# Kernel tuning notes

Hardware: AMD Instinct MI355X
Metric: run time of the kernel (lower is better)

## Reference

```python
import jax, jax.numpy as jnp
import numpy as np

B, C, H, W = 32, 384, 64, 64
M, R = 64, 16  # token_count, factor_r


def setup_inputs() -> dict:
    key = jax.random.key(0)
    k1, k2, k3, k4 = jax.random.split(key, 4)
    x = jax.random.normal(k1, (B, C, H, W), dtype=jnp.float32)
    # 1x1 conv == per-pixel linear map C -> R
    Vw = jax.random.normal(k2, (R, C), dtype=jnp.float32) * (1.0 / np.sqrt(C))
    Vb = jax.random.normal(k3, (R,), dtype=jnp.float32) * 0.01
    U = jax.random.normal(k4, (M, R), dtype=jnp.float32) * 0.02
    return {"x": x, "Vw": Vw, "Vb": Vb, "U": U}


def reference(x, Vw, Vb, U):
    b, c, h, w = x.shape
    n = h * w
    x_flat = x.reshape(b, c, n)                       # [B,C,N]
    # 1x1 conv projection: [B,R,N]
    V = jnp.einsum('rc,bcn->brn', Vw, x_flat) + Vb[None, :, None]
    # low-rank bilinear logits: [B,M,N]
    L = jnp.einsum('mr,brn->bmn', U, V)
    # softmax over token dim (axis=1), matching F.softmax(L, dim=1)
    S = jax.nn.softmax(L, axis=1)
    # pooled tokens: [B,C,M]
    T = jnp.einsum('bcn,bmn->bcm', x_flat, S)
    return (T, S)
```

## Files before the change

kernel.cpp:

```cpp
#include <hip/hip_runtime.h>
#include <hip/hip_bf16.h>

#define B_ 32
#define C_ 384
#define N_ 4096
#define M_ 64
#define R_ 16

typedef __attribute__((ext_vector_type(8))) short short8;
typedef __attribute__((ext_vector_type(4))) float f32x4;
typedef __attribute__((ext_vector_type(4))) int i32x4;

static __device__ __forceinline__ unsigned short f2bf(float f) {
    union { float f; unsigned u; } v; v.f = f;
    unsigned r = v.u + 0x7fffu + ((v.u >> 16) & 1u);
    return (unsigned short)(r >> 16);
}

__global__ __launch_bounds__(256) void k_w2(
    const float* __restrict__ Vw, const float* __restrict__ Vb,
    const float* __restrict__ U, unsigned short* __restrict__ W2,
    float* __restrict__ b2)
{
    __shared__ float vws[16 * 384];
    __shared__ float vbs[16];
    const int t = threadIdx.x;

    #pragma unroll
    for (int j = 0; j < 6; ++j)
        ((float4*)vws)[t + j * 256] = ((const float4*)Vw)[t + j * 256];
    if (t < 16) vbs[t] = Vb[t];
    __syncthreads();

    const int m  = blockIdx.x * 8 + (t >> 5);
    const int cg = t & 31;
    float u[R_];
    #pragma unroll
    for (int r = 0; r < R_; ++r) u[r] = U[m * R_ + r];
    if (cg == 0) {
        float a = 0.f;
        #pragma unroll
        for (int r = 0; r < R_; ++r) a = fmaf(u[r], vbs[r], a);
        b2[m] = a;
    }
    #pragma unroll
    for (int j = 0; j < 6; ++j) {
        const int c = cg * 2 + j * 64;
        float a0 = 0.f, a1 = 0.f;
        #pragma unroll
        for (int r = 0; r < R_; ++r) {
            float2 vv = *(const float2*)(vws + r * C_ + c);
            a0 = fmaf(u[r], vv.x, a0);
            a1 = fmaf(u[r], vv.y, a1);
        }
        unsigned pk = (unsigned)f2bf(a0) | ((unsigned)f2bf(a1) << 16);
        *(unsigned*)&W2[m * C_ + c] = pk;
    }
}

__global__ __launch_bounds__(512, 2) void k_fused(
    const float* __restrict__ x, const unsigned short* __restrict__ W2,
    const float* __restrict__ b2g, float* __restrict__ S, float* __restrict__ T)
{
    __shared__ unsigned short xcn[C_ * 128];
    __shared__ unsigned short xts[2][128][68];
    __shared__ unsigned short slds[M_ * 128];
    __shared__ float wred[2][4][128];

    const int t    = threadIdx.x;
    const int lane = t & 63;
    const int col  = lane & 15;
    const int q    = lane >> 4;
    const int w    = t >> 6;
    const int g    = w >> 1;
    const int h    = w & 1;

    const int b  = blockIdx.x >> 3;
    const int nq = blockIdx.x & 7;

    short8 af1[12];
    #pragma unroll
    for (int kk = 0; kk < 12; ++kk)
        af1[kk] = *(const short8*)(W2 + (g * 16 + col) * C_ + kk * 32 + q * 8);

    float bias[4];
    #pragma unroll
    for (int r = 0; r < 4; ++r) bias[r] = b2g[g * 16 + q * 4 + r];

    f32x4 acc2[3][4];
    #pragma unroll
    for (int ci = 0; ci < 3; ++ci)
        #pragma unroll
        for (int mt = 0; mt < 4; ++mt) acc2[ci][mt] = (f32x4){0.f, 0.f, 0.f, 0.f};

    const float* xb = x + (size_t)b * C_ * N_ + nq * 512 + 2 * lane;

    float2 xv[3][8];

    auto ISSUE = [&](float2 (&dst)[8], int subp, int kcp) {
        const float* xp = xb + (size_t)(kcp * 64 + w * 8) * N_ + subp * 128;
        #pragma unroll
        for (int i = 0; i < 8; ++i)
            dst[i] = *(const float2*)(xp + (size_t)i * N_);
    };

    auto CONVERT = [&](float2 (&v)[8], int kcp, int buf) {
        unsigned short bx[8], by[8];
        #pragma unroll
        for (int i = 0; i < 8; ++i) { bx[i] = f2bf(v[i].x); by[i] = f2bf(v[i].y); }
        #pragma unroll
        for (int i = 0; i < 8; ++i) {
            int c = kcp * 64 + w * 8 + i;
            unsigned pk = (unsigned)bx[i] | ((unsigned)by[i] << 16);
            *(unsigned*)((char*)xcn + c * 256 + ((lane * 4) ^ ((c & 7) << 4))) = pk;
        }
        i32x4 pa, pb;
        #pragma unroll
        for (int j = 0; j < 4; ++j) {
            pa[j] = (int)((unsigned)bx[2 * j] | ((unsigned)bx[2 * j + 1] << 16));
            pb[j] = (int)((unsigned)by[2 * j] | ((unsigned)by[2 * j + 1] << 16));
        }
        *(i32x4*)&xts[buf][2 * lane][w * 8]     = pa;
        *(i32x4*)&xts[buf][2 * lane + 1][w * 8] = pb;
    };

    ISSUE(xv[0], 0, 0);
    ISSUE(xv[1], 0, 1);
    ISSUE(xv[2], 0, 2);

    for (int sub = 0; sub < 4; ++sub) {
        f32x4 acc1[4];
        #pragma unroll
        for (int nt = 0; nt < 4; ++nt) acc1[nt] = (f32x4){0.f, 0.f, 0.f, 0.f};

        CONVERT(xv[0], 0, 0);
        __syncthreads();

        #pragma unroll
        for (int kc = 0; kc < 6; ++kc) {
            if (kc < 5) CONVERT(xv[(kc + 1) % 3], kc + 1, (kc + 1) & 1);
            if (kc < 3)          ISSUE(xv[kc % 3], sub, kc + 3);
            else if (sub < 3)    ISSUE(xv[kc % 3], sub + 1, kc - 3);

            #pragma unroll
            for (int ks = 0; ks < 2; ++ks) {
                short8 bfr[4];
                #pragma unroll
                for (int nt = 0; nt < 4; ++nt)
                    bfr[nt] = *(const short8*)&xts[kc & 1][h * 64 + nt * 16 + col][ks * 32 + q * 8];
                #pragma unroll
                for (int nt = 0; nt < 4; ++nt)
                    acc1[nt] = __builtin_amdgcn_mfma_f32_16x16x32_bf16(
                        af1[kc * 2 + ks], bfr[nt], acc1[nt], 0, 0, 0);
            }
            __syncthreads();
        }

        float mxl[4];
        #pragma unroll
        for (int nt = 0; nt < 4; ++nt) {
            float mx = -3.4e38f;
            #pragma unroll
            for (int r = 0; r < 4; ++r) {
                float vv = acc1[nt][r] + bias[r];
                acc1[nt][r] = vv;
                mx = fmaxf(mx, vv);
            }
            mx = fmaxf(mx, __shfl_xor(mx, 16, 64));
            mx = fmaxf(mx, __shfl_xor(mx, 32, 64));
            float s = 0.f;
            #pragma unroll
            for (int r = 0; r < 4; ++r) {
                float e = __expf(acc1[nt][r] - mx);
                acc1[nt][r] = e;
                s += e;
            }
            s += __shfl_xor(s, 16, 64);
            s += __shfl_xor(s, 32, 64);
            mxl[nt] = mx;
            if (q == 0) {
                int n = h * 64 + nt * 16 + col;
                wred[0][g][n] = mx;
                wred[1][g][n] = s;
            }
        }
        __syncthreads();

        float scl[4];
        #pragma unroll
        for (int nt = 0; nt < 4; ++nt) {
            int n = h * 64 + nt * 16 + col;
            float m0 = wred[0][0][n], m1 = wred[0][1][n];
            float m2 = wred[0][2][n], m3 = wred[0][3][n];
            float M  = fmaxf(fmaxf(m0, m1), fmaxf(m2, m3));
            float tot = wred[1][0][n] * __expf(m0 - M) + wred[1][1][n] * __expf(m1 - M)
                      + wred[1][2][n] * __expf(m2 - M) + wred[1][3][n] * __expf(m3 - M);
            scl[nt] = __expf(mxl[nt] - M) / tot;
        }

        float* Sp = S + (size_t)(b * M_ + g * 16 + q * 4) * N_ + nq * 512 + sub * 128;
        #pragma unroll
        for (int nt = 0; nt < 4; ++nt) {
            int n = h * 64 + nt * 16 + col;
            #pragma unroll
            for (int r = 0; r < 4; ++r) {
                float p = acc1[nt][r] * scl[nt];
                Sp[(size_t)r * N_ + n] = p;
                int m = g * 16 + q * 4 + r;
                *(unsigned short*)((char*)slds + m * 256 + ((2 * n) ^ ((m & 7) << 4))) = f2bf(p);
            }
        }
        __syncthreads();

        #pragma unroll
        for (int ks = 0; ks < 4; ++ks) {
            short8 a2[3], bsf[4];
            #pragma unroll
            for (int ci = 0; ci < 3; ++ci) {
                int c = w * 48 + ci * 16 + col;
                a2[ci] = *(const short8*)((char*)xcn + c * 256 +
                                          ((ks * 64 + q * 16) ^ ((c & 7) << 4)));
            }
            #pragma unroll
            for (int mt = 0; mt < 4; ++mt) {
                int m = mt * 16 + col;
                bsf[mt] = *(const short8*)((char*)slds + m * 256 +
                                           ((ks * 64 + q * 16) ^ ((m & 7) << 4)));
            }
            #pragma unroll
            for (int ci = 0; ci < 3; ++ci)
                #pragma unroll
                for (int mt = 0; mt < 4; ++mt)
                    acc2[ci][mt] = __builtin_amdgcn_mfma_f32_16x16x32_bf16(
                        a2[ci], bsf[mt], acc2[ci][mt], 0, 0, 0);
        }
        __syncthreads();
    }

    float* Tb = T + (size_t)b * C_ * M_;
    #pragma unroll
    for (int ci = 0; ci < 3; ++ci) {
        int c = w * 48 + ci * 16 + q * 4;
        #pragma unroll
        for (int mt = 0; mt < 4; ++mt)
            #pragma unroll
            for (int r = 0; r < 4; ++r)
                atomicAdd(&Tb[(size_t)(c + r) * M_ + mt * 16 + col], acc2[ci][mt][r]);
    }
}

extern "C" void kernel_launch(void* const* d_in, const int* in_sizes, int n_in,
                              void* d_out, int out_size, void* d_ws, size_t ws_size,
                              hipStream_t stream) {
    const float* x  = (const float*)d_in[0];
    const float* Vw = (const float*)d_in[1];
    const float* Vb = (const float*)d_in[2];
    const float* U  = (const float*)d_in[3];
    float* T = (float*)d_out;
    float* S = (float*)d_out + (size_t)B_ * C_ * M_;

    unsigned short* W2 = (unsigned short*)d_ws;
    float* b2 = (float*)((char*)d_ws + 64 * 384 * 2);

    hipMemsetAsync(T, 0, (size_t)B_ * C_ * M_ * sizeof(float), stream);
    k_w2<<<dim3(8), dim3(256), 0, stream>>>(Vw, Vb, U, W2, b2);
    k_fused<<<dim3(256), dim3(512), 0, stream>>>(x, W2, b2, S, T);
}
```

Before: 310.5 us.

## Halve pixel tile per block and double grid for higher occupancy

Each block now covers 256 pixels in sub-tiles of 64 instead of 512 in sub-tiles of 128, and the grid doubles to 512 blocks. Launch bounds ask for 4 blocks per SM instead of 2. The W2 fragments are reloaded from global or cache on every k-chunk rather than held in registers, and the x prefetch drops from triple to double buffering with a sync on every chunk. The goal is lower LDS and register use per block so more waves fit and latency is hidden, at the cost of more global W2 loads, more barriers and more T atomics.

```diff
diff --git a/kernel.cpp b/kernel.cpp
--- a/kernel.cpp
+++ b/kernel.cpp
@@ -58,30 +58,27 @@
     }
 }
 
-__global__ __launch_bounds__(512, 2) void k_fused(
+__global__ __launch_bounds__(512, 4) void k_fused(
     const float* __restrict__ x, const unsigned short* __restrict__ W2,
     const float* __restrict__ b2g, float* __restrict__ S, float* __restrict__ T)
 {
-    __shared__ unsigned short xcn[C_ * 128];
-    __shared__ unsigned short xts[2][128][68];
-    __shared__ unsigned short slds[M_ * 128];
-    __shared__ float wred[2][4][128];
+    __shared__ unsigned short xcn[C_ * 64];
+    __shared__ unsigned short xts[2][64][72];
+    __shared__ unsigned short slds[M_ * 64];
+    __shared__ float wred[2][4][64];
 
     const int t    = threadIdx.x;
     const int lane = t & 63;
     const int col  = lane & 15;
     const int q    = lane >> 4;
+    const int l31  = lane & 31;
+    const int l5   = lane >> 5;
     const int w    = t >> 6;
     const int g    = w >> 1;
     const int h    = w & 1;
 
-    const int b  = blockIdx.x >> 3;
-    const int nq = blockIdx.x & 7;
-
-    short8 af1[12];
-    #pragma unroll
-    for (int kk = 0; kk < 12; ++kk)
-        af1[kk] = *(const short8*)(W2 + (g * 16 + col) * C_ + kk * 32 + q * 8);
+    const int b  = blockIdx.x >> 4;
+    const int nq = blockIdx.x & 15;
 
     float bias[4];
     #pragma unroll
@@ -93,72 +90,72 @@
         #pragma unroll
         for (int mt = 0; mt < 4; ++mt) acc2[ci][mt] = (f32x4){0.f, 0.f, 0.f, 0.f};
 
-    const float* xb = x + (size_t)b * C_ * N_ + nq * 512 + 2 * lane;
-
-    float2 xv[3][8];
-
-    auto ISSUE = [&](float2 (&dst)[8], int subp, int kcp) {
-        const float* xp = xb + (size_t)(kcp * 64 + w * 8) * N_ + subp * 128;
-        #pragma unroll
-        for (int i = 0; i < 8; ++i)
-            dst[i] = *(const float2*)(xp + (size_t)i * N_);
+    const float* xb = x + (size_t)b * C_ * N_ + nq * 256 + 2 * l31;
+
+    float2 xv[2][4];
+
+    auto ISSUE = [&](float2 (&dst)[4], int subp, int kcp) {
+        const float* xp = xb + (size_t)(kcp * 64 + w * 8 + l5 * 4) * N_ + subp * 64;
+        #pragma unroll
+        for (int j = 0; j < 4; ++j)
+            dst[j] = *(const float2*)(xp + (size_t)j * N_);
     };
 
-    auto CONVERT = [&](float2 (&v)[8], int kcp, int buf) {
-        unsigned short bx[8], by[8];
-        #pragma unroll
-        for (int i = 0; i < 8; ++i) { bx[i] = f2bf(v[i].x); by[i] = f2bf(v[i].y); }
-        #pragma unroll
-        for (int i = 0; i < 8; ++i) {
-            int c = kcp * 64 + w * 8 + i;
-            unsigned pk = (unsigned)bx[i] | ((unsigned)by[i] << 16);
-            *(unsigned*)((char*)xcn + c * 256 + ((lane * 4) ^ ((c & 7) << 4))) = pk;
-        }
-        i32x4 pa, pb;
+    auto CONVERT = [&](float2 (&v)[4], int kcp, int buf) {
+        unsigned short bx[4], by[4];
+        #pragma unroll
+        for (int j = 0; j < 4; ++j) { bx[j] = f2bf(v[j].x); by[j] = f2bf(v[j].y); }
         #pragma unroll
         for (int j = 0; j < 4; ++j) {
-            pa[j] = (int)((unsigned)bx[2 * j] | ((unsigned)bx[2 * j + 1] << 16));
-            pb[j] = (int)((unsigned)by[2 * j] | ((unsigned)by[2 * j + 1] << 16));
-        }
-        *(i32x4*)&xts[buf][2 * lane][w * 8]     = pa;
-        *(i32x4*)&xts[buf][2 * lane + 1][w * 8] = pb;
+            int c = kcp * 64 + w * 8 + l5 * 4 + j;
+            unsigned pk = (unsigned)bx[j] | ((unsigned)by[j] << 16);
+            *(unsigned*)((char*)xcn + c * 128 + ((4 * l31) ^ ((c & 7) << 4))) = pk;
+        }
+        int cl = w * 8 + l5 * 4;
+        int2 pa, pb;
+        pa.x = (int)((unsigned)bx[0] | ((unsigned)bx[1] << 16));
+        pa.y = (int)((unsigned)bx[2] | ((unsigned)bx[3] << 16));
+        pb.x = (int)((unsigned)by[0] | ((unsigned)by[1] << 16));
+        pb.y = (int)((unsigned)by[2] | ((unsigned)by[3] << 16));
+        *(int2*)&xts[buf][2 * l31][cl]     = pa;
+        *(int2*)&xts[buf][2 * l31 + 1][cl] = pb;
     };
 
     ISSUE(xv[0], 0, 0);
-    ISSUE(xv[1], 0, 1);
-    ISSUE(xv[2], 0, 2);
 
     for (int sub = 0; sub < 4; ++sub) {
-        f32x4 acc1[4];
-        #pragma unroll
-        for (int nt = 0; nt < 4; ++nt) acc1[nt] = (f32x4){0.f, 0.f, 0.f, 0.f};
-
-        CONVERT(xv[0], 0, 0);
-        __syncthreads();
+        f32x4 acc1[2];
+        acc1[0] = (f32x4){0.f, 0.f, 0.f, 0.f};
+        acc1[1] = (f32x4){0.f, 0.f, 0.f, 0.f};
 
         #pragma unroll
         for (int kc = 0; kc < 6; ++kc) {
-            if (kc < 5) CONVERT(xv[(kc + 1) % 3], kc + 1, (kc + 1) & 1);
-            if (kc < 3)          ISSUE(xv[kc % 3], sub, kc + 3);
-            else if (sub < 3)    ISSUE(xv[kc % 3], sub + 1, kc - 3);
+            if (kc < 5)       ISSUE(xv[(kc + 1) & 1], sub, kc + 1);
+            else if (sub < 3) ISSUE(xv[0], sub + 1, 0);
+
+            CONVERT(xv[kc & 1], kc, kc & 1);
+            __syncthreads();
+
+            const unsigned short* wp = W2 + (g * 16 + col) * C_ + kc * 64 + q * 8;
+            short8 af0 = *(const short8*)(wp);
+            short8 af1 = *(const short8*)(wp + 32);
 
             #pragma unroll
             for (int ks = 0; ks < 2; ++ks) {
-                short8 bfr[4];
+                short8 bfr[2];
                 #pragma unroll
-                for (int nt = 0; nt < 4; ++nt)
-                    bfr[nt] = *(const short8*)&xts[kc & 1][h * 64 + nt * 16 + col][ks * 32 + q * 8];
+                for (int nt = 0; nt < 2; ++nt)
+                    bfr[nt] = *(const short8*)&xts[kc & 1][h * 32 + nt * 16 + col][ks * 32 + q * 8];
                 #pragma unroll
-                for (int nt = 0; nt < 4; ++nt)
+                for (int nt = 0; nt < 2; ++nt)
                     acc1[nt] = __builtin_amdgcn_mfma_f32_16x16x32_bf16(
-                        af1[kc * 2 + ks], bfr[nt], acc1[nt], 0, 0, 0);
-            }
-            __syncthreads();
-        }
-
-        float mxl[4];
-        #pragma unroll
-        for (int nt = 0; nt < 4; ++nt) {
+                        ks ? af1 : af0, bfr[nt], acc1[nt], 0, 0, 0);
+            }
+        }
+
+        float mxl[2], scl[2];
+        #pragma unroll
+        for (int nt = 0; nt < 2; ++nt) {
             float mx = -3.4e38f;
             #pragma unroll
             for (int r = 0; r < 4; ++r) {
@@ -179,17 +176,16 @@
             s += __shfl_xor(s, 32, 64);
             mxl[nt] = mx;
             if (q == 0) {
-                int n = h * 64 + nt * 16 + col;
+                int n = h * 32 + nt * 16 + col;
                 wred[0][g][n] = mx;
                 wred[1][g][n] = s;
             }
         }
         __syncthreads();
 
-        float scl[4];
-        #pragma unroll
-        for (int nt = 0; nt < 4; ++nt) {
-            int n = h * 64 + nt * 16 + col;
+        #pragma unroll
+        for (int nt = 0; nt < 2; ++nt) {
+            int n = h * 32 + nt * 16 + col;
             float m0 = wred[0][0][n], m1 = wred[0][1][n];
             float m2 = wred[0][2][n], m3 = wred[0][3][n];
             float M  = fmaxf(fmaxf(m0, m1), fmaxf(m2, m3));
@@ -198,33 +194,33 @@
             scl[nt] = __expf(mxl[nt] - M) / tot;
         }
 
-        float* Sp = S + (size_t)(b * M_ + g * 16 + q * 4) * N_ + nq * 512 + sub * 128;
-        #pragma unroll
-        for (int nt = 0; nt < 4; ++nt) {
-            int n = h * 64 + nt * 16 + col;
+        float* Sp = S + (size_t)(b * M_ + g * 16 + q * 4) * N_ + nq * 256 + sub * 64;
+        #pragma unroll
+        for (int nt = 0; nt < 2; ++nt) {
+            int n = h * 32 + nt * 16 + col;
             #pragma unroll
             for (int r = 0; r < 4; ++r) {
                 float p = acc1[nt][r] * scl[nt];
                 Sp[(size_t)r * N_ + n] = p;
                 int m = g * 16 + q * 4 + r;
-                *(unsigned short*)((char*)slds + m * 256 + ((2 * n) ^ ((m & 7) << 4))) = f2bf(p);
+                *(unsigned short*)((char*)slds + m * 128 + ((2 * n) ^ ((m & 7) << 4))) = f2bf(p);
             }
         }
         __syncthreads();
 
         #pragma unroll
-        for (int ks = 0; ks < 4; ++ks) {
+        for (int ks = 0; ks < 2; ++ks) {
             short8 a2[3], bsf[4];
             #pragma unroll
             for (int ci = 0; ci < 3; ++ci) {
                 int c = w * 48 + ci * 16 + col;
-                a2[ci] = *(const short8*)((char*)xcn + c * 256 +
+                a2[ci] = *(const short8*)((char*)xcn + c * 128 +
                                           ((ks * 64 + q * 16) ^ ((c & 7) << 4)));
             }
             #pragma unroll
             for (int mt = 0; mt < 4; ++mt) {
                 int m = mt * 16 + col;
-                bsf[mt] = *(const short8*)((char*)slds + m * 256 +
+                bsf[mt] = *(const short8*)((char*)slds + m * 128 +
                                            ((ks * 64 + q * 16) ^ ((m & 7) << 4)));
             }
             #pragma unroll
@@ -264,5 +260,5 @@
 
     hipMemsetAsync(T, 0, (size_t)B_ * C_ * M_ * sizeof(float), stream);
     k_w2<<<dim3(8), dim3(256), 0, stream>>>(Vw, Vb, U, W2, b2);
-    k_fused<<<dim3(256), dim3(512), 0, stream>>>(x, W2, b2, S, T);
-}
+    k_fused<<<dim3(512), dim3(512), 0, stream>>>(x, W2, b2, S, T);
+}
```

New measurement: 378.2 us. 1.22x slower.
